# Kernel optimization log

Hardware: AMD Instinct MI355X
Metric: run time of the kernel (lower is better)

## Reference

```python
import jax, jax.numpy as jnp
import numpy as np

NUM_HEADS = 8
NUM_LEVELS = 4
NUM_POINTS = 8
SPATIAL_SHAPES = np.array([[92, 160], [46, 80], [23, 40], [12, 20]], dtype=np.int64)


def _bilinear_sample(val_hw, loc, Hl, Wl):
    """val_hw: (bs, heads, H*W, d); loc: (bs, nq, heads, P, 2) in [0,1].
    Matches torch grid_sample(bilinear, zeros padding, align_corners=False)
    applied to grid = 2*loc - 1, i.e. pixel coords x = loc_x*W - 0.5.
    Returns (bs, heads, nq, P, d)."""
    x = loc[..., 0] * Wl - 0.5
    y = loc[..., 1] * Hl - 0.5
    x0 = jnp.floor(x)
    y0 = jnp.floor(y)
    wx = (x - x0).transpose(0, 2, 1, 3)  # (bs, heads, nq, P)
    wy = (y - y0).transpose(0, 2, 1, 3)
    x0i = x0.astype(jnp.int32).transpose(0, 2, 1, 3)
    y0i = y0.astype(jnp.int32).transpose(0, 2, 1, 3)

    def gather(ix, iy):
        valid = ((ix >= 0) & (ix < Wl) & (iy >= 0) & (iy < Hl)).astype(val_hw.dtype)
        idx = jnp.clip(iy, 0, Hl - 1) * Wl + jnp.clip(ix, 0, Wl - 1)  # (bs,heads,nq,P)
        b, h, nq, P = idx.shape
        g = jnp.take_along_axis(val_hw, idx.reshape(b, h, nq * P, 1), axis=2)
        return g.reshape(b, h, nq, P, -1) * valid[..., None]

    return (gather(x0i, y0i) * ((1 - wx) * (1 - wy))[..., None]
            + gather(x0i + 1, y0i) * (wx * (1 - wy))[..., None]
            + gather(x0i, y0i + 1) * ((1 - wx) * wy)[..., None]
            + gather(x0i + 1, y0i + 1) * (wx * wy)[..., None])


def setup_inputs() -> dict:
    key = jax.random.key(0)
    ks = jax.random.split(key, 10)
    C = 256
    bs, nq = 2, 10000
    nv = int((SPATIAL_SHAPES[:, 0] * SPATIAL_SHAPES[:, 1]).sum())  # 19560
    s = 1.0 / np.sqrt(C)
    return {
        "query": jax.random.normal(ks[0], (bs, nq, C), dtype=jnp.float32),
        "value": jax.random.normal(ks[1], (bs, nv, C), dtype=jnp.float32),
        "reference_points": jax.random.uniform(ks[2], (bs, nq, 4, 2), dtype=jnp.float32),
        "spatial_shapes": SPATIAL_SHAPES,
        "W_value": jax.random.normal(ks[3], (C, C), dtype=jnp.float32) * s,
        "b_value": jnp.zeros((C,), dtype=jnp.float32),
        "W_off": jax.random.normal(ks[4], (C, NUM_HEADS * NUM_LEVELS * NUM_POINTS * 2), dtype=jnp.float32) * 0.01,
        "b_off": jax.random.normal(ks[5], (NUM_HEADS * NUM_LEVELS * NUM_POINTS * 2,), dtype=jnp.float32) * 0.1,
        "W_attn": jax.random.normal(ks[6], (C, NUM_HEADS * NUM_LEVELS * NUM_POINTS), dtype=jnp.float32) * s,
        "b_attn": jnp.zeros((NUM_HEADS * NUM_LEVELS * NUM_POINTS,), dtype=jnp.float32),
    }


def reference(query, value, reference_points, spatial_shapes,
              W_value, b_value, W_off, b_off, W_attn, b_attn):
    bs, nq, C = query.shape
    NH, NL, NP = NUM_HEADS, NUM_LEVELS, NUM_POINTS
    d = C // NH
    Z = reference_points.shape[2]  # num_Z_anchors
    shapes_np = np.asarray(spatial_shapes)  # static host-side shapes

    # value / offset / attention projections
    v = (value @ W_value + b_value).reshape(bs, -1, NH, d)
    off = (query @ W_off + b_off).reshape(bs, nq, NH, NL, NP, 2)
    attn = jax.nn.softmax((query @ W_attn + b_attn).reshape(bs, nq, NH, NL * NP), axis=-1)
    attn = attn.reshape(bs, nq, NH, NL, NP)

    # normalize offsets by (W, H) per level and add to reference points
    norm = jnp.stack([spatial_shapes[:, 1], spatial_shapes[:, 0]], -1).astype(query.dtype)  # (NL, 2)
    off = off / norm[None, None, None, :, None, :]
    off = off.reshape(bs, nq, NH, NL, NP // Z, Z, 2)
    loc = reference_points[:, :, None, None, None, :, :] + off  # (bs,nq,NH,NL,NP//Z,Z,2)
    loc = loc.reshape(bs, nq, NH, NL, NP, 2)

    out = jnp.zeros((bs, NH, nq, d), dtype=query.dtype)
    start = 0
    for l in range(NL):
        Hl, Wl = int(shapes_np[l, 0]), int(shapes_np[l, 1])
        v_l = v[:, start:start + Hl * Wl].transpose(0, 2, 1, 3)  # (bs, NH, H*W, d)
        start += Hl * Wl
        sampled = _bilinear_sample(v_l, loc[:, :, :, l], Hl, Wl)  # (bs,NH,nq,NP,d)
        out = out + jnp.einsum('bhqpd,bqhp->bhqd', sampled, attn[:, :, :, l])
    return out.transpose(0, 2, 1, 3).reshape(bs, nq, NH * d)
```

## Files before the change

kernel.cpp:

```cpp
#include <hip/hip_runtime.h>
#include <math.h>

#define NH 8
#define NL 4
#define NP 8
#define CDIM 256
#define NQ 10000
#define BS 2
#define NV 19560

__constant__ int LVL_H[NL]     = {92, 46, 23, 12};
__constant__ int LVL_W[NL]     = {160, 80, 40, 20};
__constant__ int LVL_START[NL] = {0, 14720, 18400, 19320};

typedef __attribute__((ext_vector_type(8))) short short8;
typedef __attribute__((ext_vector_type(4))) float f32x4;
typedef __attribute__((ext_vector_type(2))) _Float16 half2v;
typedef __attribute__((ext_vector_type(4))) _Float16 half4v;

__device__ __forceinline__ unsigned short f2bf(float f) {
    unsigned int u = __float_as_uint(f);
    u += 0x7fffu + ((u >> 16) & 1u);
    return (unsigned short)(u >> 16);
}

__device__ __forceinline__ unsigned f2h_dup(float f) {
    const unsigned short h = __builtin_bit_cast(unsigned short, (_Float16)f);
    return (unsigned)h | ((unsigned)h << 16);
}

__global__ __launch_bounds__(256) void prep_all(
    const float* __restrict__ value, const float* __restrict__ query,
    const float* __restrict__ Wv,
    const float* __restrict__ Woff, const float* __restrict__ boff,
    const float* __restrict__ Wattn, const float* __restrict__ battn,
    unsigned short* __restrict__ valuebf, unsigned short* __restrict__ querybf,
    unsigned short* __restrict__ BvalT, unsigned short* __restrict__ BcatT,
    float* __restrict__ biascat)
{
    const int bid = blockIdx.x;
    const int t   = threadIdx.x;
    if (bid < 9780) {
        const int i = bid * 256 + t;
        const float4 f = ((const float4*)value)[i];
        ushort4 o;
        o.x = f2bf(f.x); o.y = f2bf(f.y); o.z = f2bf(f.z); o.w = f2bf(f.w);
        ((ushort4*)valuebf)[i] = o;
    } else if (bid < 14780) {
        const int i = (bid - 9780) * 256 + t;
        const float4 f = ((const float4*)query)[i];
        ushort4 o;
        o.x = f2bf(f.x); o.y = f2bf(f.y); o.z = f2bf(f.z); o.w = f2bf(f.w);
        ((ushort4*)querybf)[i] = o;
    } else {
        const int n = bid - 14780;
        if (n < 256) {
            BvalT[n * 256 + t] = f2bf(Wv[t * 256 + n]);
        } else if (n < 1024) {
            const int m = n - 256;
            const float v = (m < 512) ? Woff[t * 512 + m]
                                      : Wattn[t * 256 + (m - 512)];
            BcatT[m * 256 + t] = f2bf(v);
        } else {
            #pragma unroll
            for (int s = 0; s < 3; s++) {
                const int i = s * 256 + t;
                biascat[i] = (i < 512) ? boff[i] : battn[i - 512];
            }
        }
    }
}

#define AST 130
__global__ __launch_bounds__(256) void gemm_all(
    const unsigned short* __restrict__ valuebf,
    const unsigned short* __restrict__ BvalT,
    const float* __restrict__ b_value, _Float16* __restrict__ vproj,
    const unsigned short* __restrict__ querybf,
    const unsigned short* __restrict__ BcatT,
    const float* __restrict__ biascat, _Float16* __restrict__ offcat)
{
    __shared__ short8 Al[4 * AST];
    __shared__ short8 Bl[4 * AST];

    const int bid = blockIdx.x;
    const bool modeV = bid < 612;

    const unsigned short* A;
    const unsigned short* Bt;
    const float* bias;
    int M, N, rowBase, colBase;
    if (modeV) {
        A = valuebf; Bt = BvalT; bias = b_value;
        M = BS * NV; N = 256;
        rowBase = (bid >> 1) * 128; colBase = (bid & 1) * 128;
    } else {
        const int b2 = bid - 612;
        A = querybf; Bt = BcatT; bias = biascat;
        M = BS * NQ; N = 768;
        rowBase = (b2 / 6) * 128; colBase = (b2 % 6) * 128;
    }

    const int t = threadIdx.x;
    const int w  = t >> 6;
    const int l  = t & 63;
    const int wm = (w >> 1) * 64;
    const int wn = (w & 1) * 64;
    const int row16 = l & 15;
    const int kg    = l >> 4;

    const int sr = t >> 1;
    const int sh = t & 1;

    f32x4 acc[4][4] = {};

    for (int k0 = 0; k0 < 256; k0 += 32) {
        {
            const int grow = rowBase + sr;
            short8 v0 = {}, v1 = {};
            if (grow < M) {
                const unsigned short* ap = A + (size_t)grow * 256 + k0 + sh * 16;
                v0 = *(const short8*)ap;
                v1 = *(const short8*)(ap + 8);
            }
            Al[(sh * 2 + 0) * AST + sr] = v0;
            Al[(sh * 2 + 1) * AST + sr] = v1;
        }
        {
            const unsigned short* bp = Bt + (size_t)(colBase + sr) * 256 + k0 + sh * 16;
            Bl[(sh * 2 + 0) * AST + sr] = *(const short8*)bp;
            Bl[(sh * 2 + 1) * AST + sr] = *(const short8*)(bp + 8);
        }
        __syncthreads();

        short8 af[4], bfr[4];
        #pragma unroll
        for (int i = 0; i < 4; i++) af[i] = Al[kg * AST + wm + i * 16 + row16];
        #pragma unroll
        for (int j = 0; j < 4; j++) bfr[j] = Bl[kg * AST + wn + j * 16 + row16];
        #pragma unroll
        for (int i = 0; i < 4; i++)
            #pragma unroll
            for (int j = 0; j < 4; j++)
                acc[i][j] = __builtin_amdgcn_mfma_f32_16x16x32_bf16(
                    bfr[j], af[i], acc[i][j], 0, 0, 0);
        __syncthreads();
    }

    const int m16 = l & 15;
    const int q4  = (l >> 4) * 4;
    #pragma unroll
    for (int i = 0; i < 4; i++) {
        const int row = rowBase + wm + i * 16 + m16;
        if (row >= M) continue;
        #pragma unroll
        for (int j = 0; j < 4; j++) {
            const int col0 = colBase + wn + j * 16 + q4;
            const float4 bv = *(const float4*)&bias[col0];
            half4v o;
            o[0] = (_Float16)(acc[i][j][0] + bv.x);
            o[1] = (_Float16)(acc[i][j][1] + bv.y);
            o[2] = (_Float16)(acc[i][j][2] + bv.z);
            o[3] = (_Float16)(acc[i][j][3] + bv.w);
            _Float16* dst;
            if (modeV) {
                const int b   = (row >= NV) ? 1 : 0;
                const int pix = row - b * NV;
                const int h   = col0 >> 5;
                const int ch  = col0 & 31;
                dst = vproj + ((size_t)(b * NH + h) * NV + pix) * 32 + ch;
            } else {
                dst = offcat + (size_t)row * 768 + col0;
            }
            *(half4v*)dst = o;
        }
    }
}

__global__ __launch_bounds__(256, 8) void sample_kernel(
    const _Float16* __restrict__ vproj,
    const _Float16* __restrict__ offcat,
    const float* __restrict__ refpts,
    float* __restrict__ out)
{
    const int bid = blockIdx.x;
    const int h   = bid & 7;
    const int g   = bid >> 3;
    const int b   = g & 1;
    const int q0  = (g >> 1) * 8;
    const int t   = threadIdx.x;

    __shared__ uint2 desc[8 * 64 * 2];

    const int qi = t >> 5, j = t & 31;
    const int qrow = b * NQ + q0 + qi;

    {
        const int lv = j >> 3, p = j & 7;

        const float logit = (float)offcat[(size_t)qrow * 768 + 512 + h * 32 + j];
        const float e = __expf(logit);
        float ssum = e;
        #pragma unroll
        for (int s = 16; s > 0; s >>= 1) ssum += __shfl_xor(ssum, s, 32);
        const float aw = e / ssum;

        const int Wl = LVL_W[lv], Hl = LVL_H[lv], st = LVL_START[lv];
        const uint oxy = *(const uint*)(offcat + (size_t)qrow * 768 + h * 64 + j * 2);
        const float offx = (float)__builtin_bit_cast(half2v, oxy)[0];
        const float offy = (float)__builtin_bit_cast(half2v, oxy)[1];

        const int z = p & 3;
        const float rx = refpts[((size_t)qrow * 4 + z) * 2];
        const float ry = refpts[((size_t)qrow * 4 + z) * 2 + 1];

        const float x = fmaf(rx, (float)Wl, offx) - 0.5f;
        const float y = fmaf(ry, (float)Hl, offy) - 0.5f;
        const float x0f = floorf(x), y0f = floorf(y);
        const float wx = x - x0f, wy = y - y0f;
        const int x0 = (int)x0f, y0 = (int)y0f;

        const int xb = min(max(x0, 0), Wl - 2);
        const float wl = (x0 >= 0 && x0 < Wl)          ? (1.f - wx) : 0.f;
        const float wr = (x0 + 1 >= 0 && x0 + 1 < Wl)  ? wx         : 0.f;
        const float wA = (x0 == xb) ? wl : ((x0 + 1 == xb) ? wr : 0.f);
        const float wB = (x0 == xb) ? wr : ((x0 == xb + 1) ? wl : 0.f);

        #pragma unroll
        for (int r = 0; r < 2; r++) {
            const int yy = y0 + r;
            const float rwv = (yy >= 0 && yy < Hl)
                            ? (r ? wy : (1.f - wy)) * aw : 0.f;
            const int iy = min(max(yy, 0), Hl - 1);
            const unsigned base = (unsigned)((st + iy * Wl + xb) * 64);
            const int d = qi * 64 + j * 2 + r;
            uint2 d0, d1;
            d0.x = base;      d0.y = f2h_dup(wA * rwv);
            d1.x = base + 64; d1.y = f2h_dup(wB * rwv);
            desc[d * 2 + 0] = d0;
            desc[d * 2 + 1] = d1;
        }
    }
    __syncthreads();

    const int lane = t & 31;
    const int grp  = lane >> 3;
    const int pix  = (lane >> 2) & 1;
    const int chq  = lane & 3;

    const char* slab = (const char*)(vproj + (size_t)(b * NH + h) * NV * 32);
    const unsigned laneoff = (unsigned)(chq * 16);
    const uint2* dq = &desc[(qi * 64) * 2 + pix];

    half2v a0 = {}, a1 = {}, a2 = {}, a3 = {};
    #pragma unroll
    for (int i0 = 0; i0 < 16; i0 += 4) {
        uint2 d4[4];
        #pragma unroll
        for (int u = 0; u < 4; u++)
            d4[u] = dq[((i0 + u) * 4 + grp) * 2];
        uint4 v4[4];
        #pragma unroll
        for (int u = 0; u < 4; u++)
            v4[u] = *(const uint4*)(slab + (d4[u].x + laneoff));
        #pragma unroll
        for (int u = 0; u < 4; u++) {
            const half2v wv = __builtin_bit_cast(half2v, d4[u].y);
            a0 += wv * __builtin_bit_cast(half2v, v4[u].x);
            a1 += wv * __builtin_bit_cast(half2v, v4[u].y);
            a2 += wv * __builtin_bit_cast(half2v, v4[u].z);
            a3 += wv * __builtin_bit_cast(half2v, v4[u].w);
        }
    }

    #pragma unroll
    for (int s = 4; s <= 16; s <<= 1) {
        a0 += __builtin_bit_cast(half2v,
              __shfl_xor(__builtin_bit_cast(unsigned, a0), s, 32));
        a1 += __builtin_bit_cast(half2v,
              __shfl_xor(__builtin_bit_cast(unsigned, a1), s, 32));
        a2 += __builtin_bit_cast(half2v,
              __shfl_xor(__builtin_bit_cast(unsigned, a2), s, 32));
        a3 += __builtin_bit_cast(half2v,
              __shfl_xor(__builtin_bit_cast(unsigned, a3), s, 32));
    }

    if ((lane & 0x1C) == 0) {
        float* op = out + (size_t)qrow * 256 + h * 32 + chq * 8;
        *(float4*)op = make_float4((float)a0[0], (float)a0[1],
                                   (float)a1[0], (float)a1[1]);
        *(float4*)(op + 4) = make_float4((float)a2[0], (float)a2[1],
                                         (float)a3[0], (float)a3[1]);
    }
}

extern "C" void kernel_launch(void* const* d_in, const int* in_sizes, int n_in,
                              void* d_out, int out_size, void* d_ws, size_t ws_size,
                              hipStream_t stream)
{
    const float* query   = (const float*)d_in[0];
    const float* value   = (const float*)d_in[1];
    const float* refpts  = (const float*)d_in[2];
    const float* W_value = (const float*)d_in[4];
    const float* b_value = (const float*)d_in[5];
    const float* W_off   = (const float*)d_in[6];
    const float* b_off   = (const float*)d_in[7];
    const float* W_attn  = (const float*)d_in[8];
    const float* b_attn  = (const float*)d_in[9];

    char* ws = (char*)d_ws;
    _Float16*       vproj   = (_Float16*)(ws);
    unsigned short* valuebf = (unsigned short*)(ws + 20029440);
    unsigned short* querybf = (unsigned short*)(ws + 40058880);
    _Float16*       offcat  = (_Float16*)(ws + 50298880);
    unsigned short* BvalT   = (unsigned short*)(ws + 81018880);
    unsigned short* BcatT   = (unsigned short*)(ws + 81149952);
    float*          biascat = (float*)(ws + 81543168);

    const dim3 blk(256);

    prep_all<<<dim3(15805), blk, 0, stream>>>(
        value, query, W_value, W_off, b_off, W_attn, b_attn,
        valuebf, querybf, BvalT, BcatT, biascat);

    gemm_all<<<dim3(1554), blk, 0, stream>>>(
        valuebf, BvalT, b_value, vproj,
        querybf, BcatT, biascat, offcat);

    sample_kernel<<<dim3(BS * NQ), blk, 0, stream>>>(
        vproj, offcat, refpts, (float*)d_out);
}
```

Baseline: 215.5 us.

## Fuse value bf16 conversion into GEMM loads and restructure sampling descriptors

Drops the separate pass that converts the value tensor to bf16 in the prep kernel. The GEMM now reads fp32 value directly and converts to bf16 while staging tiles into shared memory, saving a full write and re-read of a ~20MB intermediate. It also changes the sampling kernel's shared descriptor layout to a padded per-query stride with uint4 stores, and issues 8 gathers per batch instead of 4 for more memory-level parallelism. The cost is wider fp32 global loads in the GEMM and possibly higher register pressure in the sampler.

```diff
diff --git a/kernel.cpp b/kernel.cpp
--- a/kernel.cpp
+++ b/kernel.cpp
@@ -30,30 +30,24 @@
 }
 
 __global__ __launch_bounds__(256) void prep_all(
-    const float* __restrict__ value, const float* __restrict__ query,
+    const float* __restrict__ query,
     const float* __restrict__ Wv,
     const float* __restrict__ Woff, const float* __restrict__ boff,
     const float* __restrict__ Wattn, const float* __restrict__ battn,
-    unsigned short* __restrict__ valuebf, unsigned short* __restrict__ querybf,
+    unsigned short* __restrict__ querybf,
     unsigned short* __restrict__ BvalT, unsigned short* __restrict__ BcatT,
     float* __restrict__ biascat)
 {
     const int bid = blockIdx.x;
     const int t   = threadIdx.x;
-    if (bid < 9780) {
+    if (bid < 5000) {
         const int i = bid * 256 + t;
-        const float4 f = ((const float4*)value)[i];
-        ushort4 o;
-        o.x = f2bf(f.x); o.y = f2bf(f.y); o.z = f2bf(f.z); o.w = f2bf(f.w);
-        ((ushort4*)valuebf)[i] = o;
-    } else if (bid < 14780) {
-        const int i = (bid - 9780) * 256 + t;
         const float4 f = ((const float4*)query)[i];
         ushort4 o;
         o.x = f2bf(f.x); o.y = f2bf(f.y); o.z = f2bf(f.z); o.w = f2bf(f.w);
         ((ushort4*)querybf)[i] = o;
     } else {
-        const int n = bid - 14780;
+        const int n = bid - 5000;
         if (n < 256) {
             BvalT[n * 256 + t] = f2bf(Wv[t * 256 + n]);
         } else if (n < 1024) {
@@ -73,7 +67,7 @@
 
 #define AST 130
 __global__ __launch_bounds__(256) void gemm_all(
-    const unsigned short* __restrict__ valuebf,
+    const float* __restrict__ valueF,
     const unsigned short* __restrict__ BvalT,
     const float* __restrict__ b_value, _Float16* __restrict__ vproj,
     const unsigned short* __restrict__ querybf,
@@ -86,17 +80,16 @@
     const int bid = blockIdx.x;
     const bool modeV = bid < 612;
 
-    const unsigned short* A;
     const unsigned short* Bt;
     const float* bias;
     int M, N, rowBase, colBase;
     if (modeV) {
-        A = valuebf; Bt = BvalT; bias = b_value;
+        Bt = BvalT; bias = b_value;
         M = BS * NV; N = 256;
         rowBase = (bid >> 1) * 128; colBase = (bid & 1) * 128;
     } else {
         const int b2 = bid - 612;
-        A = querybf; Bt = BcatT; bias = biascat;
+        Bt = BcatT; bias = biascat;
         M = BS * NQ; N = 768;
         rowBase = (b2 / 6) * 128; colBase = (b2 % 6) * 128;
     }
@@ -118,10 +111,29 @@
         {
             const int grow = rowBase + sr;
             short8 v0 = {}, v1 = {};
-            if (grow < M) {
-                const unsigned short* ap = A + (size_t)grow * 256 + k0 + sh * 16;
-                v0 = *(const short8*)ap;
-                v1 = *(const short8*)(ap + 8);
+            if (modeV) {
+                if (grow < M) {
+                    const float* ap = valueF + (size_t)grow * 256 + k0 + sh * 16;
+                    float va[16];
+                    #pragma unroll
+                    for (int jj = 0; jj < 4; jj++) {
+                        const float4 f = *(const float4*)(ap + jj * 4);
+                        va[jj*4+0]=f.x; va[jj*4+1]=f.y;
+                        va[jj*4+2]=f.z; va[jj*4+3]=f.w;
+                    }
+                    #pragma unroll
+                    for (int e = 0; e < 8; e++) {
+                        v0[e] = (short)f2bf(va[e]);
+                        v1[e] = (short)f2bf(va[8 + e]);
+                    }
+                }
+            } else {
+                if (grow < M) {
+                    const unsigned short* ap =
+                        querybf + (size_t)grow * 256 + k0 + sh * 16;
+                    v0 = *(const short8*)ap;
+                    v1 = *(const short8*)(ap + 8);
+                }
             }
             Al[(sh * 2 + 0) * AST + sr] = v0;
             Al[(sh * 2 + 1) * AST + sr] = v1;
@@ -190,7 +202,7 @@
     const int q0  = (g >> 1) * 8;
     const int t   = threadIdx.x;
 
-    __shared__ uint2 desc[8 * 64 * 2];
+    __shared__ uint2 desc[8 * 136];
 
     const int qi = t >> 5, j = t & 31;
     const int qrow = b * NQ + q0 + qi;
@@ -233,12 +245,10 @@
                             ? (r ? wy : (1.f - wy)) * aw : 0.f;
             const int iy = min(max(yy, 0), Hl - 1);
             const unsigned base = (unsigned)((st + iy * Wl + xb) * 64);
-            const int d = qi * 64 + j * 2 + r;
-            uint2 d0, d1;
-            d0.x = base;      d0.y = f2h_dup(wA * rwv);
-            d1.x = base + 64; d1.y = f2h_dup(wB * rwv);
-            desc[d * 2 + 0] = d0;
-            desc[d * 2 + 1] = d1;
+            uint4 dd;
+            dd.x = base;      dd.y = f2h_dup(wA * rwv);
+            dd.z = base + 64; dd.w = f2h_dup(wB * rwv);
+            *(uint4*)&desc[qi * 136 + (j * 2 + r) * 2] = dd;
         }
     }
     __syncthreads();
@@ -250,26 +260,27 @@
 
     const char* slab = (const char*)(vproj + (size_t)(b * NH + h) * NV * 32);
     const unsigned laneoff = (unsigned)(chq * 16);
-    const uint2* dq = &desc[(qi * 64) * 2 + pix];
+    const uint* dqw = (const uint*)&desc[qi * 136 + grp * 2 + pix];
 
     half2v a0 = {}, a1 = {}, a2 = {}, a3 = {};
     #pragma unroll
-    for (int i0 = 0; i0 < 16; i0 += 4) {
-        uint2 d4[4];
-        #pragma unroll
-        for (int u = 0; u < 4; u++)
-            d4[u] = dq[((i0 + u) * 4 + grp) * 2];
-        uint4 v4[4];
-        #pragma unroll
-        for (int u = 0; u < 4; u++)
-            v4[u] = *(const uint4*)(slab + (d4[u].x + laneoff));
-        #pragma unroll
-        for (int u = 0; u < 4; u++) {
-            const half2v wv = __builtin_bit_cast(half2v, d4[u].y);
-            a0 += wv * __builtin_bit_cast(half2v, v4[u].x);
-            a1 += wv * __builtin_bit_cast(half2v, v4[u].y);
-            a2 += wv * __builtin_bit_cast(half2v, v4[u].z);
-            a3 += wv * __builtin_bit_cast(half2v, v4[u].w);
+    for (int half = 0; half < 2; half++) {
+        unsigned addr[8];
+        #pragma unroll
+        for (int u = 0; u < 8; u++)
+            addr[u] = dqw[(half * 8 + u) * 16] + laneoff;
+        uint4 v[8];
+        #pragma unroll
+        for (int u = 0; u < 8; u++)
+            v[u] = *(const uint4*)(slab + addr[u]);
+        #pragma unroll
+        for (int u = 0; u < 8; u++) {
+            const half2v wv = __builtin_bit_cast(half2v,
+                                  dqw[(half * 8 + u) * 16 + 1]);
+            a0 += wv * __builtin_bit_cast(half2v, v[u].x);
+            a1 += wv * __builtin_bit_cast(half2v, v[u].y);
+            a2 += wv * __builtin_bit_cast(half2v, v[u].z);
+            a3 += wv * __builtin_bit_cast(half2v, v[u].w);
         }
     }
 
@@ -310,21 +321,20 @@
 
     char* ws = (char*)d_ws;
     _Float16*       vproj   = (_Float16*)(ws);
-    unsigned short* valuebf = (unsigned short*)(ws + 20029440);
-    unsigned short* querybf = (unsigned short*)(ws + 40058880);
-    _Float16*       offcat  = (_Float16*)(ws + 50298880);
-    unsigned short* BvalT   = (unsigned short*)(ws + 81018880);
-    unsigned short* BcatT   = (unsigned short*)(ws + 81149952);
-    float*          biascat = (float*)(ws + 81543168);
+    unsigned short* querybf = (unsigned short*)(ws + 20029440);
+    _Float16*       offcat  = (_Float16*)(ws + 30269440);
+    unsigned short* BvalT   = (unsigned short*)(ws + 60989440);
+    unsigned short* BcatT   = (unsigned short*)(ws + 61120512);
+    float*          biascat = (float*)(ws + 61513728);
 
     const dim3 blk(256);
 
-    prep_all<<<dim3(15805), blk, 0, stream>>>(
-        value, query, W_value, W_off, b_off, W_attn, b_attn,
-        valuebf, querybf, BvalT, BcatT, biascat);
+    prep_all<<<dim3(6025), blk, 0, stream>>>(
+        query, W_value, W_off, b_off, W_attn, b_attn,
+        querybf, BvalT, BcatT, biascat);
 
     gemm_all<<<dim3(1554), blk, 0, stream>>>(
-        valuebf, BvalT, b_value, vproj,
+        value, BvalT, b_value, vproj,
         querybf, BcatT, biascat, offcat);
 
     sample_kernel<<<dim3(BS * NQ), blk, 0, stream>>>(
```

Result: no change. 211.5 us (-1.9%).
